# Kernel optimization log

Measured on AMD Instinct MI355X. Metric: run time of the kernel, lower is better.

The kernel has to match this reference:

```python
import jax, jax.numpy as jnp
import numpy as np

LEAK = 0.1
EPS = 1e-5

N, C, T, V = 32, 64, 400, 27
S, IC, O = 2, 16, 64  # num_subset, inter_channels, out_channels


def _make_pe(channel, joint_num, time_len):
    pos = np.tile(np.arange(joint_num), time_len).astype(np.float32)[:, None]
    div = np.exp(np.arange(0, channel, 2).astype(np.float32) * (-(np.log(10000.0) / channel)))
    pe = np.zeros((time_len * joint_num, channel), np.float32)
    pe[:, 0::2] = np.sin(pos * div)
    pe[:, 1::2] = np.cos(pos * div)
    # (T*V, C) -> (1, C, T, V)
    return jnp.asarray(pe.reshape(time_len, joint_num, channel).transpose(2, 0, 1)[None])


def setup_inputs() -> dict:
    key = jax.random.key(0)
    ks = jax.random.split(key, 16)
    w = lambda k, shp, fan: jax.random.normal(k, shp, jnp.float32) * (1.0 / np.sqrt(fan))
    inp = {
        "x": jax.random.normal(ks[0], (N, C, T, V), jnp.float32),
        "pe": _make_pe(C, V, T),
        # in_nets: Conv2d(C, 2*S*IC, 1)
        "W_in": w(ks[1], (2 * S * IC, C), C),
        "b_in": jnp.zeros((2 * S * IC,), jnp.float32),
        "alphas": jnp.ones((1, S, 1, 1), jnp.float32),
        "att0": jnp.ones((1, S, V, V), jnp.float32) / V,
        # out_nets: Conv2d(S*C, O, 1) + BN
        "W_out": w(ks[2], (O, S * C), S * C),
        "b_out": jnp.zeros((O,), jnp.float32),
        "g_out": jnp.ones((O,), jnp.float32),
        "be_out": jnp.zeros((O,), jnp.float32),
        "m_out": jax.random.normal(ks[3], (O,), jnp.float32) * 0.1,
        "v_out": jax.random.uniform(ks[4], (O,), jnp.float32, 0.5, 1.5),
        # ff_nets: Conv2d(O, O, 1) + BN
        "W_ff": w(ks[5], (O, O), O),
        "b_ff": jnp.zeros((O,), jnp.float32),
        "g_ff": jnp.ones((O,), jnp.float32),
        "be_ff": jnp.zeros((O,), jnp.float32),
        "m_ff": jax.random.normal(ks[6], (O,), jnp.float32) * 0.1,
        "v_ff": jax.random.uniform(ks[7], (O,), jnp.float32, 0.5, 1.5),
        # out_nett: Conv2d(O, O, (3,1), pad (1,0)) + BN
        "W_t": w(ks[8], (O, O, 3, 1), O * 3),
        "b_t": jnp.zeros((O,), jnp.float32),
        "g_t": jnp.ones((O,), jnp.float32),
        "be_t": jnp.zeros((O,), jnp.float32),
        "m_t": jax.random.normal(ks[9], (O,), jnp.float32) * 0.1,
        "v_t": jax.random.uniform(ks[10], (O,), jnp.float32, 0.5, 1.5),
    }
    return inp


def _lrelu(x):
    return jnp.where(x >= 0, x, LEAK * x)


def _bn(x, g, b, m, v):
    scale = g / jnp.sqrt(v + EPS)
    return (x - m[None, :, None, None]) * scale[None, :, None, None] + b[None, :, None, None]


def _conv1x1(x, W, b):
    return jnp.einsum('oc,nctv->notv', W, x) + b[None, :, None, None]


def reference(x, pe, W_in, b_in, alphas, att0, W_out, b_out, g_out, be_out, m_out, v_out,
              W_ff, b_ff, g_ff, be_ff, m_ff, v_ff, W_t, b_t, g_t, be_t, m_t, v_t):
    n, c, t, v_ = x.shape
    s = alphas.shape[1]
    ic = W_in.shape[0] // (2 * s)
    # positional encoding on the attention-input branch only
    y = x + pe[:, :, :t]
    qk = _conv1x1(y, W_in, b_in).reshape(n, 2 * s, ic, t, v_)
    q, k = qk[:, :s], qk[:, s:]
    # atts buffer is zeros; dropout is identity in eval
    att = jnp.tanh(jnp.einsum('nsctu,nsctv->nsuv', q, k) / (ic * t)) * alphas + att0
    y = jnp.einsum('nctu,nsuv->nsctv', x, att).reshape(n, s * c, t, v_)
    y = _bn(_conv1x1(y, W_out, b_out), g_out, be_out, m_out, v_out)
    y = _lrelu(x + y)  # downs1 = identity
    yf = _bn(_conv1x1(y, W_ff, b_ff), g_ff, be_ff, m_ff, v_ff)
    y = _lrelu(x + yf)  # downs2 = identity
    z = jax.lax.conv_general_dilated(
        y, W_t, window_strides=(1, 1), padding=((1, 1), (0, 0)),
        dimension_numbers=('NCHW', 'OIHW', 'NCHW'))
    z = _bn(z + b_t[None, :, None, None], g_t, be_t, m_t, v_t)
    z = _lrelu(y + z)  # downt2 = identity
    return z
```

## Files before the change

### kernel.cpp

```cpp
#include <hip/hip_runtime.h>
#include <hip/hip_bf16.h>

typedef __hip_bfloat16 bf16;
typedef unsigned short u16;
typedef __attribute__((ext_vector_type(8))) short short8;
typedef __attribute__((ext_vector_type(4))) short s4v;
typedef __attribute__((ext_vector_type(4))) float f32x4;
typedef __attribute__((ext_vector_type(4))) unsigned int u32x4;

#define LEAK 0.1f
#define EPS_ 1e-5f
#define MFMA(a, b, c) __builtin_amdgcn_mfma_f32_16x16x32_bf16(a, b, c, 0, 0, 0)

__device__ __forceinline__ float u2f(u16 u) { return __uint_as_float(((unsigned int)u) << 16); }
__device__ __forceinline__ u16 f2u(float f) {
  bf16 h = __float2bfloat16(f);
  u16 r;
  __builtin_memcpy(&r, &h, 2);
  return r;
}
__device__ __forceinline__ f32x4 z4() { f32x4 z = {0.f, 0.f, 0.f, 0.f}; return z; }

__global__ __launch_bounds__(512, 2) void g_qk_att(
    const float* __restrict__ x, const float* __restrict__ pe,
    const float* __restrict__ W_in, const float* __restrict__ b_in,
    float* __restrict__ att)
{
  __shared__ __align__(16) u16 sB16[14 * 2 * 64 * 8];
  __shared__ __align__(16) u16 sQF[2][32][136];
  __shared__ __align__(16) u16 sKF[2][32][136];
  const int tid = threadIdx.x;
  const int w = tid >> 6, lane = tid & 63;
  const int m = lane & 15, quad = lane >> 4;
  const int ot = w & 3, g = w >> 2;
  const int n = blockIdx.y;
  const int p0 = blockIdx.x * 216;

  short8 aW[2];
#pragma unroll
  for (int kf = 0; kf < 2; ++kf) {
    short8 tt;
#pragma unroll
    for (int j = 0; j < 8; ++j)
      tt[j] = (short)f2u(W_in[(16 * ot + m) * 64 + 32 * kf + 8 * quad + j]);
    aW[kf] = tt;
  }
  float bb[4];
#pragma unroll
  for (int r = 0; r < 4; ++r) bb[r] = b_in[16 * ot + quad * 4 + r];

#pragma unroll 4
  for (int i = 0; i < 28; ++i) {
    int idx = i * 512 + tid;
    int c = idx / 224, pl = idx % 224;
    float v = 0.f;
    if (pl < 216)
      v = x[(n * 64 + c) * 10800 + p0 + pl] + pe[c * 10800 + p0 + pl];
    int tile = pl >> 4, mm = pl & 15;
    int kf = c >> 5, qq = (c >> 3) & 3, j = c & 7;
    sB16[(((tile * 2 + kf) * 64) + qq * 16 + mm) * 8 + j] = f2u(v);
  }
  __syncthreads();

  u16* dstF = (ot < 2 ? &sQF[0][0][0] : &sKF[0][0][0]) + (ot & 1) * 32 * 136;
#pragma unroll
  for (int ti = 0; ti < 7; ++ti) {
    int tile = 7 * g + ti;
    short8 b0 = *(const short8*)&sB16[((tile * 2 + 0) * 64 + lane) * 8];
    short8 b1 = *(const short8*)&sB16[((tile * 2 + 1) * 64 + lane) * 8];
    f32x4 acc = MFMA(aW[0], b0, z4());
    acc = MFMA(aW[1], b1, acc);
    int pl = tile * 16 + m;
    if (pl < 216) {
      int tl = pl / 27, u = pl - tl * 27;
      s4v pk;
#pragma unroll
      for (int reg = 0; reg < 4; ++reg) pk[reg] = (short)f2u(acc[reg] + bb[reg]);
      *(s4v*)&dstF[u * 136 + tl * 16 + quad * 4] = pk;
    }
  }
  __syncthreads();

  {
    const int s = w & 1, ut = (w >> 1) & 1, vt = w >> 2;
    f32x4 acc = z4();
#pragma unroll
    for (int ks = 0; ks < 4; ++ks) {
      short8 a = *(const short8*)&sQF[s][ut * 16 + m][ks * 32 + quad * 8];
      short8 b = *(const short8*)&sKF[s][vt * 16 + m][ks * 32 + quad * 8];
      acc = MFMA(a, b, acc);
    }
#pragma unroll
    for (int reg = 0; reg < 4; ++reg) {
      int u = ut * 16 + quad * 4 + reg, v = vt * 16 + m;
      if (u < 27 && v < 27)
        atomicAdd(&att[(n * 2 + s) * 729 + u * 27 + v], acc[reg]);
    }
  }
}

__global__ __launch_bounds__(256) void k_att_fin(
    float* __restrict__ att, const float* __restrict__ alphas,
    const float* __restrict__ att0)
{
  int i = blockIdx.x * 256 + threadIdx.x;
  if (i >= 32 * 2 * 729) return;
  int s = (i / 729) & 1;
  int r = i % 729;
  att[i] = tanhf(att[i] * (1.f / 6400.f)) * alphas[s] + att0[s * 729 + r];
}

__global__ __launch_bounds__(512, 2) void g_ab(
    const float* __restrict__ x, const float* __restrict__ att,
    const float* __restrict__ W_out, const float* __restrict__ b_out,
    const float* __restrict__ g_out, const float* __restrict__ be_out,
    const float* __restrict__ m_out, const float* __restrict__ v_out,
    u16* __restrict__ y3T)
{
  __shared__ __align__(16) float sxf[6944];
  __shared__ __align__(16) float satt[1464];
  __shared__ u32x4 sy2f[4][2][4][64];
  const int tid = threadIdx.x;
  const int w = tid >> 6, lane = tid & 63;
  const int m = lane & 15, quad = lane >> 4;
  const int ot = w & 3, g = w >> 2;
  const int n = blockIdx.y, t0 = blockIdx.x * 4;

  short8 aWo[4];
#pragma unroll
  for (int kf = 0; kf < 4; ++kf) {
    short8 tt;
#pragma unroll
    for (int j = 0; j < 8; ++j)
      tt[j] = (short)f2u(W_out[(16 * ot + m) * 128 + 32 * kf + 8 * quad + j]);
    aWo[kf] = tt;
  }
  float Ao[4], Bo[4];
#pragma unroll
  for (int reg = 0; reg < 4; ++reg) {
    int o = 16 * ot + quad * 4 + reg;
    float sc = g_out[o] * rsqrtf(v_out[o] + EPS_);
    Ao[reg] = sc;
    Bo[reg] = (b_out[o] - m_out[o]) * sc + be_out[o];
  }

  for (int i = tid; i < 1728; i += 512) {
    int c = i / 27, q = i - c * 27;
    f32x4 tv = *(const f32x4*)&x[(n * 64 + c) * 10800 + t0 * 27 + q * 4];
    *(f32x4*)&sxf[c * 108 + q * 4] = tv;
  }
  for (int i = tid; i < 1458; i += 512) satt[i] = att[n * 1458 + i];
  __syncthreads();

  short8 bAtt[4];
#pragma unroll
  for (int s = 0; s < 2; ++s)
#pragma unroll
    for (int nt = 0; nt < 2; ++nt) {
      short8 tt;
#pragma unroll
      for (int j = 0; j < 8; ++j) {
        int u = 8 * quad + j, v = 16 * nt + m;
        tt[j] = (u < 27 && v < 27) ? (short)f2u(satt[s * 729 + u * 27 + v]) : (short)0;
      }
      bAtt[s * 2 + nt] = tt;
    }

  const int q1 = quad & 1;
  const int qp = (2 * ot + (quad >> 1)) & 3;
#pragma unroll
  for (int li = 0; li < 2; ++li) {
    int tc = 2 * li + g;
    short8 ax;
#pragma unroll
    for (int j = 0; j < 8; ++j) {
      int u = quad * 8 + j;
      ax[j] = (u < 27) ? (short)f2u(sxf[(16 * ot + m) * 108 + tc * 27 + u]) : (short)0;
    }
    f32x4 acc[4];
#pragma unroll
    for (int f = 0; f < 4; ++f) acc[f] = MFMA(ax, bAtt[f], z4());
#pragma unroll
    for (int s = 0; s < 2; ++s)
#pragma unroll
      for (int nt = 0; nt < 2; ++nt) {
        f32x4 a = acc[s * 2 + nt];
        s4v pk;
#pragma unroll
        for (int reg = 0; reg < 4; ++reg) pk[reg] = (short)f2u(a[reg]);
        int kfp = 2 * s + (ot >> 1);
        *(s4v*)((u16*)&sy2f[tc][nt][kfp][qp * 16 + m] + 4 * q1) = pk;
      }
  }
  __syncthreads();
#pragma unroll
  for (int ci = 0; ci < 2; ++ci) {
    int tc = 2 * ci + g;
    int t = t0 + tc;
#pragma unroll
    for (int vt = 0; vt < 2; ++vt) {
      f32x4 a0 = z4();
#pragma unroll
      for (int kf = 0; kf < 4; ++kf) {
        short8 b = *(const short8*)&sy2f[tc][vt][kf][lane];
        a0 = MFMA(aWo[kf], b, a0);
      }
      int v = vt * 16 + m;
      if (v < 27) {
        s4v pk;
#pragma unroll
        for (int reg = 0; reg < 4; ++reg) {
          int o = 16 * ot + quad * 4 + reg;
          float r = sxf[o * 108 + tc * 27 + v] + a0[reg] * Ao[reg] + Bo[reg];
          pk[reg] = (short)f2u((r >= 0.f) ? r : LEAK * r);
        }
        *(s4v*)&y3T[(unsigned)(n * 10800 + t * 27 + v) * 64 + 16 * ot + quad * 4] = pk;
      }
    }
  }
}

__global__ __launch_bounds__(512, 2) void g_cd(
    const float* __restrict__ x, const u16* __restrict__ y3T,
    const float* __restrict__ W_ff, const float* __restrict__ b_ff,
    const float* __restrict__ g_ff, const float* __restrict__ be_ff,
    const float* __restrict__ m_ff, const float* __restrict__ v_ff,
    const float* __restrict__ W_t, const float* __restrict__ b_t,
    const float* __restrict__ g_t, const float* __restrict__ be_t,
    const float* __restrict__ m_t, const float* __restrict__ v_t,
    float* __restrict__ out)
{
  __shared__ u32x4 sy4f[10][2][2][64];
  const int tid = threadIdx.x;
  const int w = tid >> 6, lane = tid & 63;
  const int m = lane & 15, quad = lane >> 4;
  const int ot = w & 3, g = w >> 2;
  const int n = blockIdx.y, t0 = blockIdx.x * 8;

  short8 aWf[2], aWt[6];
#pragma unroll
  for (int kf = 0; kf < 2; ++kf) {
    short8 tt;
#pragma unroll
    for (int j = 0; j < 8; ++j)
      tt[j] = (short)f2u(W_ff[(16 * ot + m) * 64 + 32 * kf + 8 * quad + j]);
    aWf[kf] = tt;
  }
#pragma unroll
  for (int kf = 0; kf < 6; ++kf) {
    short8 tt;
    int dt = kf >> 1;
#pragma unroll
    for (int j = 0; j < 8; ++j) {
      int ii = 32 * (kf & 1) + 8 * quad + j;
      tt[j] = (short)f2u(W_t[((16 * ot + m) * 64 + ii) * 3 + dt]);
    }
    aWt[kf] = tt;
  }
  float Af[4], Bf[4], At[4], Bt[4];
#pragma unroll
  for (int reg = 0; reg < 4; ++reg) {
    int o = 16 * ot + quad * 4 + reg;
    float sc;
    sc = g_ff[o] * rsqrtf(v_ff[o] + EPS_); Af[reg] = sc; Bf[reg] = (b_ff[o] - m_ff[o]) * sc + be_ff[o];
    sc = g_t[o] * rsqrtf(v_t[o] + EPS_);   At[reg] = sc; Bt[reg] = (b_t[o] - m_t[o]) * sc + be_t[o];
  }

  const int q1 = quad & 1;
  const int qp = (2 * ot + (quad >> 1)) & 3;
  const int kfp = ot >> 1;
#pragma unroll
  for (int li = 0; li < 5; ++li) {
    int tl = 2 * li + g;
    int t = t0 - 1 + tl;
    if (t >= 0 && t < 400) {
      short8 yb[2][2];
      float xr[2][4];
#pragma unroll
      for (int vt = 0; vt < 2; ++vt) {
        int v = vt * 16 + m;
        unsigned p = (unsigned)(n * 10800 + t * 27 + v);
        yb[vt][0] = *(const short8*)&y3T[p * 64 + quad * 8];
        yb[vt][1] = *(const short8*)&y3T[p * 64 + 32 + quad * 8];
#pragma unroll
        for (int reg = 0; reg < 4; ++reg) {
          int o = 16 * ot + quad * 4 + reg;
          xr[vt][reg] = (v < 27) ? x[((n * 64 + o) * 400 + t) * 27 + v] : 0.f;
        }
      }
#pragma unroll
      for (int vt = 0; vt < 2; ++vt) {
        f32x4 acc = MFMA(aWf[0], yb[vt][0], z4());
        acc = MFMA(aWf[1], yb[vt][1], acc);
        s4v pk;
#pragma unroll
        for (int reg = 0; reg < 4; ++reg) {
          float r = xr[vt][reg] + acc[reg] * Af[reg] + Bf[reg];
          pk[reg] = (short)f2u((r >= 0.f) ? r : LEAK * r);
        }
        *(s4v*)((u16*)&sy4f[tl][vt][kfp][qp * 16 + m] + 4 * q1) = pk;
      }
    } else {
      s4v zz = {0, 0, 0, 0};
#pragma unroll
      for (int vt = 0; vt < 2; ++vt)
        *(s4v*)((u16*)&sy4f[tl][vt][kfp][qp * 16 + m] + 4 * q1) = zz;
    }
  }
  __syncthreads();
#pragma unroll
  for (int ci = 0; ci < 4; ++ci) {
    int tc = 2 * ci + g;
    int t = t0 + tc;
#pragma unroll
    for (int vt = 0; vt < 2; ++vt) {
      f32x4 acc = z4();
#pragma unroll
      for (int kf = 0; kf < 6; ++kf) {
        short8 b = *(const short8*)&sy4f[tc + (kf >> 1)][vt][kf & 1][lane];
        acc = MFMA(aWt[kf], b, acc);
      }
      int v = vt * 16 + m;
      if (v < 27) {
        s4v res = *(const s4v*)((const u16*)&sy4f[tc + 1][vt][kfp][qp * 16 + m] + 4 * q1);
#pragma unroll
        for (int reg = 0; reg < 4; ++reg) {
          int o = 16 * ot + quad * 4 + reg;
          float r = u2f((u16)res[reg]) + acc[reg] * At[reg] + Bt[reg];
          out[((n * 64 + o) * 400 + t) * 27 + v] = (r >= 0.f) ? r : LEAK * r;
        }
      }
    }
  }
}

extern "C" void kernel_launch(void* const* d_in, const int* in_sizes, int n_in,
                              void* d_out, int out_size, void* d_ws, size_t ws_size,
                              hipStream_t stream)
{
  const float* x      = (const float*)d_in[0];
  const float* pe     = (const float*)d_in[1];
  const float* W_in   = (const float*)d_in[2];
  const float* b_in   = (const float*)d_in[3];
  const float* alphas = (const float*)d_in[4];
  const float* att0   = (const float*)d_in[5];
  const float* W_out  = (const float*)d_in[6];
  const float* b_out  = (const float*)d_in[7];
  const float* g_out  = (const float*)d_in[8];
  const float* be_out = (const float*)d_in[9];
  const float* m_out  = (const float*)d_in[10];
  const float* v_out  = (const float*)d_in[11];
  const float* W_ff   = (const float*)d_in[12];
  const float* b_ff   = (const float*)d_in[13];
  const float* g_ff   = (const float*)d_in[14];
  const float* be_ff  = (const float*)d_in[15];
  const float* m_ff   = (const float*)d_in[16];
  const float* v_ff   = (const float*)d_in[17];
  const float* W_t    = (const float*)d_in[18];
  const float* b_t    = (const float*)d_in[19];
  const float* g_t    = (const float*)d_in[20];
  const float* be_t   = (const float*)d_in[21];
  const float* m_t    = (const float*)d_in[22];
  const float* v_t    = (const float*)d_in[23];

  float* att = (float*)d_ws;
  u16* y3T = (u16*)((char*)d_ws + (1u << 20));

  hipMemsetAsync(att, 0, 32 * 2 * 729 * sizeof(float), stream);
  g_qk_att<<<dim3(50, 32), 512, 0, stream>>>(x, pe, W_in, b_in, att);
  k_att_fin<<<dim3(183), 256, 0, stream>>>(att, alphas, att0);
  g_ab<<<dim3(100, 32), 512, 0, stream>>>(
      x, att, W_out, b_out, g_out, be_out, m_out, v_out, y3T);
  g_cd<<<dim3(50, 32), 512, 0, stream>>>(
      x, y3T, W_ff, b_ff, g_ff, be_ff, m_ff, v_ff,
      W_t, b_t, g_t, be_t, m_t, v_t, (float*)d_out);
}
```

Baseline: 404.7 us.

## Fuse attention-apply, out-conv, ff-conv and temporal conv into one kernel

Merges the g_ab and g_cd kernels into a single g_abcd kernel. Each block handles 4 time steps plus a one-step halo on each side, recomputing the halo steps so the 3-tap temporal conv can run entirely from shared memory. This removes the bf16 y3T round trip through global memory and one kernel launch. The cost is halo recomputation, about 115 KB of shared memory per block (down to one block per CU), and serial ff/temporal stages. The qk kernel's staging loop is also changed to use float4 loads of x and pe.

```diff
diff --git a/kernel.cpp b/kernel.cpp
--- a/kernel.cpp
+++ b/kernel.cpp
@@ -49,16 +49,20 @@
 #pragma unroll
   for (int r = 0; r < 4; ++r) bb[r] = b_in[16 * ot + quad * 4 + r];
 
-#pragma unroll 4
-  for (int i = 0; i < 28; ++i) {
-    int idx = i * 512 + tid;
-    int c = idx / 224, pl = idx % 224;
-    float v = 0.f;
-    if (pl < 216)
-      v = x[(n * 64 + c) * 10800 + p0 + pl] + pe[c * 10800 + p0 + pl];
-    int tile = pl >> 4, mm = pl & 15;
-    int kf = c >> 5, qq = (c >> 3) & 3, j = c & 7;
-    sB16[(((tile * 2 + kf) * 64) + qq * 16 + mm) * 8 + j] = f2u(v);
+#pragma unroll
+  for (int i = 0; i < 7; ++i) {
+    int unit = i * 512 + tid;
+    if (unit < 3456) {
+      int c = unit / 54, p4 = unit - c * 54;
+      int pl = p4 * 4;
+      f32x4 xv = *(const f32x4*)&x[(n * 64 + c) * 10800 + p0 + pl];
+      f32x4 pv = *(const f32x4*)&pe[c * 10800 + p0 + pl];
+      int kf = c >> 5, qq = (c >> 3) & 3, j = c & 7;
+      int tile = pl >> 4, mm = pl & 15;
+#pragma unroll
+      for (int e = 0; e < 4; ++e)
+        sB16[(((tile * 2 + kf) * 64) + qq * 16 + mm + e) * 8 + j] = f2u(xv[e] + pv[e]);
+    }
   }
   __syncthreads();
 
@@ -110,118 +114,11 @@
   att[i] = tanhf(att[i] * (1.f / 6400.f)) * alphas[s] + att0[s * 729 + r];
 }
 
-__global__ __launch_bounds__(512, 2) void g_ab(
+__global__ __launch_bounds__(512, 2) void g_abcd(
     const float* __restrict__ x, const float* __restrict__ att,
     const float* __restrict__ W_out, const float* __restrict__ b_out,
     const float* __restrict__ g_out, const float* __restrict__ be_out,
     const float* __restrict__ m_out, const float* __restrict__ v_out,
-    u16* __restrict__ y3T)
-{
-  __shared__ __align__(16) float sxf[6944];
-  __shared__ __align__(16) float satt[1464];
-  __shared__ u32x4 sy2f[4][2][4][64];
-  const int tid = threadIdx.x;
-  const int w = tid >> 6, lane = tid & 63;
-  const int m = lane & 15, quad = lane >> 4;
-  const int ot = w & 3, g = w >> 2;
-  const int n = blockIdx.y, t0 = blockIdx.x * 4;
-
-  short8 aWo[4];
-#pragma unroll
-  for (int kf = 0; kf < 4; ++kf) {
-    short8 tt;
-#pragma unroll
-    for (int j = 0; j < 8; ++j)
-      tt[j] = (short)f2u(W_out[(16 * ot + m) * 128 + 32 * kf + 8 * quad + j]);
-    aWo[kf] = tt;
-  }
-  float Ao[4], Bo[4];
-#pragma unroll
-  for (int reg = 0; reg < 4; ++reg) {
-    int o = 16 * ot + quad * 4 + reg;
-    float sc = g_out[o] * rsqrtf(v_out[o] + EPS_);
-    Ao[reg] = sc;
-    Bo[reg] = (b_out[o] - m_out[o]) * sc + be_out[o];
-  }
-
-  for (int i = tid; i < 1728; i += 512) {
-    int c = i / 27, q = i - c * 27;
-    f32x4 tv = *(const f32x4*)&x[(n * 64 + c) * 10800 + t0 * 27 + q * 4];
-    *(f32x4*)&sxf[c * 108 + q * 4] = tv;
-  }
-  for (int i = tid; i < 1458; i += 512) satt[i] = att[n * 1458 + i];
-  __syncthreads();
-
-  short8 bAtt[4];
-#pragma unroll
-  for (int s = 0; s < 2; ++s)
-#pragma unroll
-    for (int nt = 0; nt < 2; ++nt) {
-      short8 tt;
-#pragma unroll
-      for (int j = 0; j < 8; ++j) {
-        int u = 8 * quad + j, v = 16 * nt + m;
-        tt[j] = (u < 27 && v < 27) ? (short)f2u(satt[s * 729 + u * 27 + v]) : (short)0;
-      }
-      bAtt[s * 2 + nt] = tt;
-    }
-
-  const int q1 = quad & 1;
-  const int qp = (2 * ot + (quad >> 1)) & 3;
-#pragma unroll
-  for (int li = 0; li < 2; ++li) {
-    int tc = 2 * li + g;
-    short8 ax;
-#pragma unroll
-    for (int j = 0; j < 8; ++j) {
-      int u = quad * 8 + j;
-      ax[j] = (u < 27) ? (short)f2u(sxf[(16 * ot + m) * 108 + tc * 27 + u]) : (short)0;
-    }
-    f32x4 acc[4];
-#pragma unroll
-    for (int f = 0; f < 4; ++f) acc[f] = MFMA(ax, bAtt[f], z4());
-#pragma unroll
-    for (int s = 0; s < 2; ++s)
-#pragma unroll
-      for (int nt = 0; nt < 2; ++nt) {
-        f32x4 a = acc[s * 2 + nt];
-        s4v pk;
-#pragma unroll
-        for (int reg = 0; reg < 4; ++reg) pk[reg] = (short)f2u(a[reg]);
-        int kfp = 2 * s + (ot >> 1);
-        *(s4v*)((u16*)&sy2f[tc][nt][kfp][qp * 16 + m] + 4 * q1) = pk;
-      }
-  }
-  __syncthreads();
-#pragma unroll
-  for (int ci = 0; ci < 2; ++ci) {
-    int tc = 2 * ci + g;
-    int t = t0 + tc;
-#pragma unroll
-    for (int vt = 0; vt < 2; ++vt) {
-      f32x4 a0 = z4();
-#pragma unroll
-      for (int kf = 0; kf < 4; ++kf) {
-        short8 b = *(const short8*)&sy2f[tc][vt][kf][lane];
-        a0 = MFMA(aWo[kf], b, a0);
-      }
-      int v = vt * 16 + m;
-      if (v < 27) {
-        s4v pk;
-#pragma unroll
-        for (int reg = 0; reg < 4; ++reg) {
-          int o = 16 * ot + quad * 4 + reg;
-          float r = sxf[o * 108 + tc * 27 + v] + a0[reg] * Ao[reg] + Bo[reg];
-          pk[reg] = (short)f2u((r >= 0.f) ? r : LEAK * r);
-        }
-        *(s4v*)&y3T[(unsigned)(n * 10800 + t * 27 + v) * 64 + 16 * ot + quad * 4] = pk;
-      }
-    }
-  }
-}
-
-__global__ __launch_bounds__(512, 2) void g_cd(
-    const float* __restrict__ x, const u16* __restrict__ y3T,
     const float* __restrict__ W_ff, const float* __restrict__ b_ff,
     const float* __restrict__ g_ff, const float* __restrict__ be_ff,
     const float* __restrict__ m_ff, const float* __restrict__ v_ff,
@@ -230,108 +127,217 @@
     const float* __restrict__ m_t, const float* __restrict__ v_t,
     float* __restrict__ out)
 {
-  __shared__ u32x4 sy4f[10][2][2][64];
+  __shared__ __align__(16) char smem[115456];
+  float* sxf = (float*)smem;
+  u32x4* sy2f = (u32x4*)(smem + 41728);
+  u32x4* sy4f = (u32x4*)(smem + 41728);
+  u32x4* sy3f = (u32x4*)(smem + 41728 + 49152);
+#define IDX2(sl, nt, kfp, ln) ((((sl)*2 + (nt)) * 4 + (kfp)) * 64 + (ln))
+#define IDX3(sl, vt, kf, ln) ((((sl)*2 + (vt)) * 2 + (kf)) * 64 + (ln))
   const int tid = threadIdx.x;
   const int w = tid >> 6, lane = tid & 63;
   const int m = lane & 15, quad = lane >> 4;
   const int ot = w & 3, g = w >> 2;
-  const int n = blockIdx.y, t0 = blockIdx.x * 8;
-
-  short8 aWf[2], aWt[6];
-#pragma unroll
-  for (int kf = 0; kf < 2; ++kf) {
-    short8 tt;
-#pragma unroll
-    for (int j = 0; j < 8; ++j)
-      tt[j] = (short)f2u(W_ff[(16 * ot + m) * 64 + 32 * kf + 8 * quad + j]);
-    aWf[kf] = tt;
-  }
-#pragma unroll
-  for (int kf = 0; kf < 6; ++kf) {
-    short8 tt;
-    int dt = kf >> 1;
-#pragma unroll
-    for (int j = 0; j < 8; ++j) {
-      int ii = 32 * (kf & 1) + 8 * quad + j;
-      tt[j] = (short)f2u(W_t[((16 * ot + m) * 64 + ii) * 3 + dt]);
-    }
-    aWt[kf] = tt;
-  }
-  float Af[4], Bf[4], At[4], Bt[4];
-#pragma unroll
-  for (int reg = 0; reg < 4; ++reg) {
-    int o = 16 * ot + quad * 4 + reg;
-    float sc;
-    sc = g_ff[o] * rsqrtf(v_ff[o] + EPS_); Af[reg] = sc; Bf[reg] = (b_ff[o] - m_ff[o]) * sc + be_ff[o];
-    sc = g_t[o] * rsqrtf(v_t[o] + EPS_);   At[reg] = sc; Bt[reg] = (b_t[o] - m_t[o]) * sc + be_t[o];
-  }
+  const int n = blockIdx.y, t0 = blockIdx.x * 4;
 
   const int q1 = quad & 1;
   const int qp = (2 * ot + (quad >> 1)) & 3;
-  const int kfp = ot >> 1;
-#pragma unroll
-  for (int li = 0; li < 5; ++li) {
-    int tl = 2 * li + g;
-    int t = t0 - 1 + tl;
-    if (t >= 0 && t < 400) {
-      short8 yb[2][2];
-      float xr[2][4];
+
+  {
+    int base = t0 * 27 - 27;
+    for (int i = tid; i < 10368; i += 512) {
+      int c = i / 162, r = i - c * 162;
+      int gg = base + r;
+      sxf[c * 163 + r] = (gg >= 0 && gg < 10800) ? x[(n * 64 + c) * 10800 + gg] : 0.f;
+    }
+  }
+  short8 bAtt[4];
+#pragma unroll
+  for (int s = 0; s < 2; ++s)
+#pragma unroll
+    for (int nt = 0; nt < 2; ++nt) {
+      short8 tt;
+#pragma unroll
+      for (int j = 0; j < 8; ++j) {
+        int u = 8 * quad + j, v = 16 * nt + m;
+        tt[j] = (u < 27 && v < 27) ? (short)f2u(att[(n * 2 + s) * 729 + u * 27 + v]) : (short)0;
+      }
+      bAtt[s * 2 + nt] = tt;
+    }
+  __syncthreads();
+
+#pragma unroll
+  for (int li = 0; li < 3; ++li) {
+    int sl = 2 * li + g;
+    int t = t0 - 1 + sl;
+    if (t < 0 || t >= 400) continue;
+    short8 ax;
+#pragma unroll
+    for (int j = 0; j < 8; ++j) {
+      int u = quad * 8 + j;
+      ax[j] = (u < 27) ? (short)f2u(sxf[(16 * ot + m) * 163 + sl * 27 + u]) : (short)0;
+    }
+    f32x4 acc[4];
+#pragma unroll
+    for (int f = 0; f < 4; ++f) acc[f] = MFMA(ax, bAtt[f], z4());
+#pragma unroll
+    for (int s = 0; s < 2; ++s)
+#pragma unroll
+      for (int nt = 0; nt < 2; ++nt) {
+        f32x4 a = acc[s * 2 + nt];
+        s4v pk;
+#pragma unroll
+        for (int reg = 0; reg < 4; ++reg) pk[reg] = (short)f2u(a[reg]);
+        *(s4v*)((u16*)&sy2f[IDX2(sl, nt, 2 * s + (ot >> 1), qp * 16 + m)] + 4 * q1) = pk;
+      }
+  }
+  __syncthreads();
+
+  {
+    short8 aWo[4];
+#pragma unroll
+    for (int kf = 0; kf < 4; ++kf) {
+      short8 tt;
+#pragma unroll
+      for (int j = 0; j < 8; ++j)
+        tt[j] = (short)f2u(W_out[(16 * ot + m) * 128 + 32 * kf + 8 * quad + j]);
+      aWo[kf] = tt;
+    }
+    float Ao[4], Bo[4];
+#pragma unroll
+    for (int reg = 0; reg < 4; ++reg) {
+      int o = 16 * ot + quad * 4 + reg;
+      float sc = g_out[o] * rsqrtf(v_out[o] + EPS_);
+      Ao[reg] = sc;
+      Bo[reg] = (b_out[o] - m_out[o]) * sc + be_out[o];
+    }
+#pragma unroll
+    for (int li = 0; li < 3; ++li) {
+      int sl = 2 * li + g;
+      int t = t0 - 1 + sl;
+      if (t < 0 || t >= 400) continue;
 #pragma unroll
       for (int vt = 0; vt < 2; ++vt) {
+        f32x4 a0 = z4();
+#pragma unroll
+        for (int kf = 0; kf < 4; ++kf) {
+          short8 b = *(const short8*)&sy2f[IDX2(sl, vt, kf, lane)];
+          a0 = MFMA(aWo[kf], b, a0);
+        }
         int v = vt * 16 + m;
-        unsigned p = (unsigned)(n * 10800 + t * 27 + v);
-        yb[vt][0] = *(const short8*)&y3T[p * 64 + quad * 8];
-        yb[vt][1] = *(const short8*)&y3T[p * 64 + 32 + quad * 8];
-#pragma unroll
-        for (int reg = 0; reg < 4; ++reg) {
-          int o = 16 * ot + quad * 4 + reg;
-          xr[vt][reg] = (v < 27) ? x[((n * 64 + o) * 400 + t) * 27 + v] : 0.f;
-        }
-      }
+        if (v < 27) {
+          s4v pk;
+#pragma unroll
+          for (int reg = 0; reg < 4; ++reg) {
+            int o = 16 * ot + quad * 4 + reg;
+            float r = sxf[o * 163 + sl * 27 + v] + a0[reg] * Ao[reg] + Bo[reg];
+            pk[reg] = (short)f2u((r >= 0.f) ? r : LEAK * r);
+          }
+          *(s4v*)((u16*)&sy3f[IDX3(sl, vt, ot >> 1, qp * 16 + m)] + 4 * q1) = pk;
+        }
+      }
+    }
+  }
+  __syncthreads();
+
+  {
+    short8 aWf[2];
+#pragma unroll
+    for (int kf = 0; kf < 2; ++kf) {
+      short8 tt;
+#pragma unroll
+      for (int j = 0; j < 8; ++j)
+        tt[j] = (short)f2u(W_ff[(16 * ot + m) * 64 + 32 * kf + 8 * quad + j]);
+      aWf[kf] = tt;
+    }
+    float Af[4], Bf[4];
+#pragma unroll
+    for (int reg = 0; reg < 4; ++reg) {
+      int o = 16 * ot + quad * 4 + reg;
+      float sc = g_ff[o] * rsqrtf(v_ff[o] + EPS_);
+      Af[reg] = sc;
+      Bf[reg] = (b_ff[o] - m_ff[o]) * sc + be_ff[o];
+    }
+#pragma unroll
+    for (int li = 0; li < 3; ++li) {
+      int sl = 2 * li + g;
+      int t = t0 - 1 + sl;
+      if (t >= 0 && t < 400) {
+#pragma unroll
+        for (int vt = 0; vt < 2; ++vt) {
+          short8 yb0 = *(const short8*)&sy3f[IDX3(sl, vt, 0, lane)];
+          short8 yb1 = *(const short8*)&sy3f[IDX3(sl, vt, 1, lane)];
+          f32x4 acc = MFMA(aWf[0], yb0, z4());
+          acc = MFMA(aWf[1], yb1, acc);
+          int v = vt * 16 + m;
+          s4v pk;
+#pragma unroll
+          for (int reg = 0; reg < 4; ++reg) {
+            int o = 16 * ot + quad * 4 + reg;
+            float xr = (v < 27) ? sxf[o * 163 + sl * 27 + v] : 0.f;
+            float r = xr + acc[reg] * Af[reg] + Bf[reg];
+            pk[reg] = (short)f2u((r >= 0.f) ? r : LEAK * r);
+          }
+          *(s4v*)((u16*)&sy4f[IDX3(sl, vt, ot >> 1, qp * 16 + m)] + 4 * q1) = pk;
+        }
+      } else {
+        s4v zz = {0, 0, 0, 0};
+#pragma unroll
+        for (int vt = 0; vt < 2; ++vt)
+          *(s4v*)((u16*)&sy4f[IDX3(sl, vt, ot >> 1, qp * 16 + m)] + 4 * q1) = zz;
+      }
+    }
+  }
+  __syncthreads();
+
+  {
+    short8 aWt[6];
+#pragma unroll
+    for (int kf = 0; kf < 6; ++kf) {
+      short8 tt;
+      int dt = kf >> 1;
+#pragma unroll
+      for (int j = 0; j < 8; ++j) {
+        int ii = 32 * (kf & 1) + 8 * quad + j;
+        tt[j] = (short)f2u(W_t[((16 * ot + m) * 64 + ii) * 3 + dt]);
+      }
+      aWt[kf] = tt;
+    }
+    float At[4], Bt[4];
+#pragma unroll
+    for (int reg = 0; reg < 4; ++reg) {
+      int o = 16 * ot + quad * 4 + reg;
+      float sc = g_t[o] * rsqrtf(v_t[o] + EPS_);
+      At[reg] = sc;
+      Bt[reg] = (b_t[o] - m_t[o]) * sc + be_t[o];
+    }
+#pragma unroll
+    for (int ci = 0; ci < 2; ++ci) {
+      int tc = 2 * ci + g;
+      int t = t0 + tc;
 #pragma unroll
       for (int vt = 0; vt < 2; ++vt) {
-        f32x4 acc = MFMA(aWf[0], yb[vt][0], z4());
-        acc = MFMA(aWf[1], yb[vt][1], acc);
-        s4v pk;
-#pragma unroll
-        for (int reg = 0; reg < 4; ++reg) {
-          float r = xr[vt][reg] + acc[reg] * Af[reg] + Bf[reg];
-          pk[reg] = (short)f2u((r >= 0.f) ? r : LEAK * r);
-        }
-        *(s4v*)((u16*)&sy4f[tl][vt][kfp][qp * 16 + m] + 4 * q1) = pk;
-      }
-    } else {
-      s4v zz = {0, 0, 0, 0};
-#pragma unroll
-      for (int vt = 0; vt < 2; ++vt)
-        *(s4v*)((u16*)&sy4f[tl][vt][kfp][qp * 16 + m] + 4 * q1) = zz;
-    }
-  }
-  __syncthreads();
-#pragma unroll
-  for (int ci = 0; ci < 4; ++ci) {
-    int tc = 2 * ci + g;
-    int t = t0 + tc;
-#pragma unroll
-    for (int vt = 0; vt < 2; ++vt) {
-      f32x4 acc = z4();
-#pragma unroll
-      for (int kf = 0; kf < 6; ++kf) {
-        short8 b = *(const short8*)&sy4f[tc + (kf >> 1)][vt][kf & 1][lane];
-        acc = MFMA(aWt[kf], b, acc);
-      }
-      int v = vt * 16 + m;
-      if (v < 27) {
-        s4v res = *(const s4v*)((const u16*)&sy4f[tc + 1][vt][kfp][qp * 16 + m] + 4 * q1);
-#pragma unroll
-        for (int reg = 0; reg < 4; ++reg) {
-          int o = 16 * ot + quad * 4 + reg;
-          float r = u2f((u16)res[reg]) + acc[reg] * At[reg] + Bt[reg];
-          out[((n * 64 + o) * 400 + t) * 27 + v] = (r >= 0.f) ? r : LEAK * r;
-        }
-      }
-    }
-  }
+        f32x4 acc = z4();
+#pragma unroll
+        for (int kf = 0; kf < 6; ++kf) {
+          short8 b = *(const short8*)&sy4f[IDX3(tc + (kf >> 1), vt, kf & 1, lane)];
+          acc = MFMA(aWt[kf], b, acc);
+        }
+        int v = vt * 16 + m;
+        if (v < 27) {
+          s4v res = *(const s4v*)((const u16*)&sy4f[IDX3(tc + 1, vt, ot >> 1, qp * 16 + m)] + 4 * q1);
+#pragma unroll
+          for (int reg = 0; reg < 4; ++reg) {
+            int o = 16 * ot + quad * 4 + reg;
+            float r = u2f((u16)res[reg]) + acc[reg] * At[reg] + Bt[reg];
+            out[((n * 64 + o) * 400 + t) * 27 + v] = (r >= 0.f) ? r : LEAK * r;
+          }
+        }
+      }
+    }
+  }
+#undef IDX2
+#undef IDX3
 }
 
 extern "C" void kernel_launch(void* const* d_in, const int* in_sizes, int n_in,
@@ -364,14 +370,13 @@
   const float* v_t    = (const float*)d_in[23];
 
   float* att = (float*)d_ws;
-  u16* y3T = (u16*)((char*)d_ws + (1u << 20));
 
   hipMemsetAsync(att, 0, 32 * 2 * 729 * sizeof(float), stream);
   g_qk_att<<<dim3(50, 32), 512, 0, stream>>>(x, pe, W_in, b_in, att);
   k_att_fin<<<dim3(183), 256, 0, stream>>>(att, alphas, att0);
-  g_ab<<<dim3(100, 32), 512, 0, stream>>>(
-      x, att, W_out, b_out, g_out, be_out, m_out, v_out, y3T);
-  g_cd<<<dim3(50, 32), 512, 0, stream>>>(
-      x, y3T, W_ff, b_ff, g_ff, be_ff, m_ff, v_ff,
+  g_abcd<<<dim3(100, 32), 512, 0, stream>>>(
+      x, att,
+      W_out, b_out, g_out, be_out, m_out, v_out,
+      W_ff, b_ff, g_ff, be_ff, m_ff, v_ff,
       W_t, b_t, g_t, be_t, m_t, v_t, (float*)d_out);
 }
```

New measurement: 480.4 us. +18.7%, slower.
